# Optimization experiments

Hardware: AMD Instinct MI355X
Metric: run time of the kernel (lower is better)

## Reference

```python
import jax, jax.numpy as jnp
import numpy as np


def setup_inputs() -> dict:
    key = jax.random.key(0)
    kq, kk, kv = jax.random.split(key, 3)
    B, S, D = 16, 2048, 128
    q = jax.random.normal(kq, (B, S, D), dtype=jnp.float32)
    k = jax.random.normal(kk, (B, S, D), dtype=jnp.float32)
    v = jax.random.normal(kv, (B, S, D), dtype=jnp.float32)
    return {"q": q, "k": k, "v": v}


def reference(q, k, v):
    # scores = q @ k^T * scale  (scale = 1/sqrt(head_dim), the standard value
    # passed to this module; dropout=0.0 and attn_mask=None per defaults)
    scale = q.shape[-1] ** -0.5
    scores = jnp.einsum('bqd,bkd->bqk', q, k) * scale  # [B, S, S]
    attention = jax.nn.softmax(scores, axis=-1)
    context = jnp.einsum('bqk,bkd->bqd', attention, v)  # [B, S, D]
    return (context, attention)
```

## Files before the change

### kernel.cpp

```cpp
#include <hip/hip_runtime.h>

#define SS 2048
#define DD 128
#define NB 16
#define TM 64
#define TN 64
#define NITER (SS / TN)

typedef short bf16x8 __attribute__((ext_vector_type(8)));
typedef float f32x4 __attribute__((ext_vector_type(4)));

#define PSTRIDE 72

#define SL2E (0.08838834764831845f * 1.4426950408889634f)

__device__ __forceinline__ unsigned short f2bf(float x) {
    unsigned u = __builtin_bit_cast(unsigned, x);
    u += 0x7fffu + ((u >> 16) & 1u);
    return (unsigned short)(u >> 16);
}

__device__ __forceinline__ float fexp2(float x) {
#if __has_builtin(__builtin_amdgcn_exp2f)
    return __builtin_amdgcn_exp2f(x);
#else
    return __expf(x * 0.6931471805599453f);
#endif
}

#define LGKM0() asm volatile("s_waitcnt lgkmcnt(0)" ::: "memory")
#define BAR()   __builtin_amdgcn_s_barrier()

__global__ void prep_kernel(const float* __restrict__ k, const float* __restrict__ v,
                            unsigned short* __restrict__ kb, unsigned short* __restrict__ vt) {
    __shared__ unsigned short t[64 * 72];
    const int x = blockIdx.x, b = blockIdx.z, sb = blockIdx.y * 64;
    const int tid = threadIdx.x;
    if (x < 2) {
        const int db = x * 64;
        const int r16 = tid >> 4, c4 = (tid & 15) * 4;
        for (int i = 0; i < 4; ++i) {
            int sl = i * 16 + r16;
            float4 xx = *(const float4*)(v + ((size_t)(b * SS + sb + sl) * DD + db + c4));
            ushort4 u; u.x = f2bf(xx.x); u.y = f2bf(xx.y); u.z = f2bf(xx.z); u.w = f2bf(xx.w);
            *(ushort4*)&t[sl * 72 + c4] = u;
        }
        __syncthreads();
        for (int i = 0; i < 4; ++i) {
            int dl = i * 16 + r16;
            ushort4 u;
            u.x = t[(c4 + 0) * 72 + dl];
            u.y = t[(c4 + 1) * 72 + dl];
            u.z = t[(c4 + 2) * 72 + dl];
            u.w = t[(c4 + 3) * 72 + dl];
            *(ushort4*)(vt + ((size_t)(b * DD + db + dl) * SS + sb + c4)) = u;
        }
    } else {
        const int c0 = (x - 2) * 64;
        for (int i = 0; i < 4; ++i) {
            int e = i * 1024 + tid * 4;
            int r = e >> 6, c = e & 63;
            size_t off = (size_t)(b * SS + sb + r) * DD + c0 + c;
            float4 xx = *(const float4*)(k + off);
            ushort4 u; u.x = f2bf(xx.x); u.y = f2bf(xx.y); u.z = f2bf(xx.z); u.w = f2bf(xx.w);
            *(ushort4*)(kb + off) = u;
        }
    }
}

__global__ __launch_bounds__(512, 4)
void attn_kernel(const float* __restrict__ q,
                 const unsigned short* __restrict__ kb,
                 const unsigned short* __restrict__ vt,
                 float* __restrict__ attn, float* __restrict__ ctx) {
    __shared__ unsigned short P_lds[2][TM * PSTRIDE];
    __shared__ float rs_lds[TM];
    __shared__ float inv_lds[TM];

    const int tid = threadIdx.x;
    const int lane = tid & 63, w = tid >> 6;
    const int wm = w >> 2, wn = w & 3;
    const int l15 = lane & 15, quad = lane >> 4;

    const int bid = blockIdx.x;
    const int bb = ((bid & 7) << 1) | ((bid >> 3) & 1);
    const int q0 = (bid >> 4) * TM;

    if (tid < TM) rs_lds[tid] = 0.0f;

    bf16x8 qf[2][4];
    {
        const float* qg = q + ((size_t)(bb * SS + q0 + wm * 32 + l15)) * DD + quad * 8;
        for (int mi = 0; mi < 2; ++mi)
            for (int kk = 0; kk < 4; ++kk) {
                float4 a = *(const float4*)(qg + mi * 16 * DD + kk * 32);
                float4 b = *(const float4*)(qg + mi * 16 * DD + kk * 32 + 4);
                bf16x8 f;
                f[0] = (short)f2bf(a.x); f[1] = (short)f2bf(a.y);
                f[2] = (short)f2bf(a.z); f[3] = (short)f2bf(a.w);
                f[4] = (short)f2bf(b.x); f[5] = (short)f2bf(b.y);
                f[6] = (short)f2bf(b.z); f[7] = (short)f2bf(b.w);
                qf[mi][kk] = f;
            }
    }

    const unsigned short* kgb = kb + (size_t)bb * SS * DD;
    const unsigned short* vgb = vt + (size_t)bb * DD * SS;

    float rs[8];
    for (int j = 0; j < 8; ++j) rs[j] = 0.0f;
    {
        const unsigned short* kp = kgb + (size_t)(wn * 16 + l15) * DD + quad * 8;
#pragma unroll 2
        for (int it = 0; it < NITER; ++it) {
            f32x4 a0 = (f32x4){0.f, 0.f, 0.f, 0.f};
            f32x4 a1 = (f32x4){0.f, 0.f, 0.f, 0.f};
#pragma unroll
            for (int kk = 0; kk < 4; ++kk) {
                bf16x8 kf = *(const bf16x8*)(kp + kk * 32);
                a0 = __builtin_amdgcn_mfma_f32_16x16x32_bf16(qf[0][kk], kf, a0, 0, 0, 0);
                a1 = __builtin_amdgcn_mfma_f32_16x16x32_bf16(qf[1][kk], kf, a1, 0, 0, 0);
            }
#pragma unroll
            for (int r = 0; r < 4; ++r) {
                rs[r]     += fexp2(a0[r] * SL2E);
                rs[4 + r] += fexp2(a1[r] * SL2E);
            }
            kp += TN * DD;
        }
    }

#pragma unroll
    for (int j = 0; j < 8; ++j) {
        float s = rs[j];
        s += __shfl_xor(s, 1, 64);
        s += __shfl_xor(s, 2, 64);
        s += __shfl_xor(s, 4, 64);
        s += __shfl_xor(s, 8, 64);
        rs[j] = s;
    }
    __syncthreads();
    if (l15 == 0)
        for (int mi = 0; mi < 2; ++mi)
            for (int r = 0; r < 4; ++r)
                atomicAdd(&rs_lds[wm * 32 + mi * 16 + quad * 4 + r], rs[mi * 4 + r]);
    __syncthreads();
    if (tid < TM) inv_lds[tid] = 1.0f / rs_lds[tid];
    __syncthreads();
    float inv[2][4];
    for (int mi = 0; mi < 2; ++mi)
        for (int r = 0; r < 4; ++r)
            inv[mi][r] = inv_lds[wm * 32 + mi * 16 + quad * 4 + r];

    f32x4 cacc[2][2];
    for (int mi = 0; mi < 2; ++mi)
        for (int ni = 0; ni < 2; ++ni) cacc[mi][ni] = (f32x4){0.f, 0.f, 0.f, 0.f};

    float* ab = attn + (size_t)bb * SS * SS
              + (size_t)(q0 + wm * 32) * SS + (wn * 16 + l15);
    const unsigned short* kp0 = kgb + (size_t)(wn * 16 + l15) * DD + quad * 8;
    const unsigned short* vfp = vgb + (size_t)(wn * 32 + l15) * SS + quad * 8;

    bf16x8 kf[4];
#pragma unroll
    for (int kk = 0; kk < 4; ++kk) kf[kk] = *(const bf16x8*)(kp0 + kk * 32);
    const unsigned short* kpn = kp0 + (size_t)TN * DD;

    for (int it = 0; it < NITER; ++it) {
        const int k0 = it * TN;

        f32x4 acc[2];
        acc[0] = (f32x4){0.f, 0.f, 0.f, 0.f};
        acc[1] = (f32x4){0.f, 0.f, 0.f, 0.f};
        __builtin_amdgcn_s_setprio(1);
#pragma unroll
        for (int kk = 0; kk < 4; ++kk) {
            acc[0] = __builtin_amdgcn_mfma_f32_16x16x32_bf16(qf[0][kk], kf[kk], acc[0], 0, 0, 0);
            acc[1] = __builtin_amdgcn_mfma_f32_16x16x32_bf16(qf[1][kk], kf[kk], acc[1], 0, 0, 0);
        }
        __builtin_amdgcn_s_setprio(0);

        if (it < NITER - 1) {
#pragma unroll
            for (int kk = 0; kk < 4; ++kk) kf[kk] = *(const bf16x8*)(kpn + kk * 32);
            kpn += (size_t)TN * DD;
        }

        bf16x8 bv[2][2];
#pragma unroll
        for (int kk = 0; kk < 2; ++kk)
#pragma unroll
            for (int ni = 0; ni < 2; ++ni)
                bv[kk][ni] = *(const bf16x8*)(vfp + (size_t)(ni * 16) * SS + k0 + kk * 32);

        unsigned short* pw = &P_lds[it & 1][0];
#pragma unroll
        for (int mi = 0; mi < 2; ++mi)
#pragma unroll
            for (int r = 0; r < 4; ++r) {
                float p = fexp2(acc[mi][r] * SL2E) * inv[mi][r];
                __builtin_nontemporal_store(p, ab + (size_t)((mi * 16 + quad * 4 + r) * SS) + k0);
                pw[(wm * 32 + mi * 16 + quad * 4 + r) * PSTRIDE + wn * 16 + l15] = f2bf(p);
            }

        LGKM0();
        BAR();

        __builtin_amdgcn_s_setprio(1);
#pragma unroll
        for (int kk = 0; kk < 2; ++kk) {
            bf16x8 af0 = *(const bf16x8*)&pw[(wm * 32 +  0 + l15) * PSTRIDE + kk * 32 + quad * 8];
            bf16x8 af1 = *(const bf16x8*)&pw[(wm * 32 + 16 + l15) * PSTRIDE + kk * 32 + quad * 8];
            cacc[0][0] = __builtin_amdgcn_mfma_f32_16x16x32_bf16(af0, bv[kk][0], cacc[0][0], 0, 0, 0);
            cacc[1][0] = __builtin_amdgcn_mfma_f32_16x16x32_bf16(af1, bv[kk][0], cacc[1][0], 0, 0, 0);
            cacc[0][1] = __builtin_amdgcn_mfma_f32_16x16x32_bf16(af0, bv[kk][1], cacc[0][1], 0, 0, 0);
            cacc[1][1] = __builtin_amdgcn_mfma_f32_16x16x32_bf16(af1, bv[kk][1], cacc[1][1], 0, 0, 0);
        }
        __builtin_amdgcn_s_setprio(0);
    }

    float* cg = ctx + ((size_t)(bb * SS) + q0) * DD;
#pragma unroll
    for (int mi = 0; mi < 2; ++mi)
#pragma unroll
        for (int ni = 0; ni < 2; ++ni)
#pragma unroll
            for (int r = 0; r < 4; ++r) {
                int row = wm * 32 + mi * 16 + quad * 4 + r;
                int col = wn * 32 + ni * 16 + l15;
                __builtin_nontemporal_store(cacc[mi][ni][r], cg + (size_t)row * DD + col);
            }
}

extern "C" void kernel_launch(void* const* d_in, const int* in_sizes, int n_in,
                              void* d_out, int out_size, void* d_ws, size_t ws_size,
                              hipStream_t stream) {
    const float* q = (const float*)d_in[0];
    const float* k = (const float*)d_in[1];
    const float* v = (const float*)d_in[2];
    float* ctx = (float*)d_out;
    float* attn = ctx + (size_t)NB * SS * DD;

    unsigned short* kb = (unsigned short*)d_ws;
    unsigned short* vt = kb + (size_t)NB * SS * DD;

    prep_kernel<<<dim3(4, SS / 64, NB), 256, 0, stream>>>(k, v, kb, vt);
    attn_kernel<<<dim3((SS / TM) * NB), 512, 0, stream>>>(q, kb, vt, attn, ctx);
}
```

Baseline: 455.2 us.

## Stage K and V tiles into swizzled LDS via async global-to-LDS loads

K tiles, and V tiles in the second pass, are now cooperatively prefetched into XOR-swizzled shared memory buffers with global_load_lds. This replaces per-wave direct global loads, which duplicated K reads across the two wm wave rows. It adds a multi-buffered ring with vmcnt waits and an extra barrier per iteration. LDS use rises to about 64KB of K/V buffers, which may cut occupancy below the launch bound of 4 blocks. The P buffer also drops from double to single buffering.

```diff
diff --git a/kernel.cpp b/kernel.cpp
--- a/kernel.cpp
+++ b/kernel.cpp
@@ -28,8 +28,36 @@
 #endif
 }
 
-#define LGKM0() asm volatile("s_waitcnt lgkmcnt(0)" ::: "memory")
-#define BAR()   __builtin_amdgcn_s_barrier()
+#define LGKM0()    asm volatile("s_waitcnt lgkmcnt(0)" ::: "memory")
+#define VMCNT(n)   asm volatile("s_waitcnt vmcnt(" #n ")" ::: "memory")
+#define BAR()      __builtin_amdgcn_s_barrier()
+#define MEMFENCE() asm volatile("" ::: "memory")
+
+__device__ __forceinline__ void gld16(unsigned short* lds, const unsigned short* g) {
+    __builtin_amdgcn_global_load_lds(
+        (const __attribute__((address_space(1))) void*)g,
+        (__attribute__((address_space(3))) void*)lds, 16, 0, 0);
+}
+
+__device__ __forceinline__ void stage_k(unsigned short* buf, const unsigned short* kg, int tid) {
+#pragma unroll
+    for (int c = 0; c < 2; ++c) {
+        int e = c * 512 + tid;
+        int r = e >> 4;
+        int co = (e & 15) ^ (r & 7);
+        gld16(buf + e * 8, kg + (size_t)r * DD + co * 8);
+    }
+}
+
+__device__ __forceinline__ void stage_v(unsigned short* buf, const unsigned short* vg, int tid) {
+#pragma unroll
+    for (int c = 0; c < 2; ++c) {
+        int e = c * 512 + tid;
+        int r = e >> 3;
+        int co = (e & 7) ^ (r & 7);
+        gld16(buf + e * 8, vg + (size_t)r * SS + co * 8);
+    }
+}
 
 __global__ void prep_kernel(const float* __restrict__ k, const float* __restrict__ v,
                             unsigned short* __restrict__ kb, unsigned short* __restrict__ vt) {
@@ -73,7 +101,8 @@
                  const unsigned short* __restrict__ kb,
                  const unsigned short* __restrict__ vt,
                  float* __restrict__ attn, float* __restrict__ ctx) {
-    __shared__ unsigned short P_lds[2][TM * PSTRIDE];
+    __shared__ unsigned short KV[4][64 * 128];
+    __shared__ unsigned short P_lds[TM * PSTRIDE];
     __shared__ float rs_lds[TM];
     __shared__ float inv_lds[TM];
 
@@ -81,6 +110,7 @@
     const int lane = tid & 63, w = tid >> 6;
     const int wm = w >> 2, wn = w & 3;
     const int l15 = lane & 15, quad = lane >> 4;
+    const int sx = (l15 & 7) << 4;
 
     const int bid = blockIdx.x;
     const int bb = ((bid & 7) << 1) | ((bid >> 3) & 1);
@@ -106,28 +136,35 @@
 
     const unsigned short* kgb = kb + (size_t)bb * SS * DD;
     const unsigned short* vgb = vt + (size_t)bb * DD * SS;
+    const int rK = wn * 16 + l15;
 
     float rs[8];
     for (int j = 0; j < 8; ++j) rs[j] = 0.0f;
-    {
-        const unsigned short* kp = kgb + (size_t)(wn * 16 + l15) * DD + quad * 8;
-#pragma unroll 2
-        for (int it = 0; it < NITER; ++it) {
-            f32x4 a0 = (f32x4){0.f, 0.f, 0.f, 0.f};
-            f32x4 a1 = (f32x4){0.f, 0.f, 0.f, 0.f};
-#pragma unroll
-            for (int kk = 0; kk < 4; ++kk) {
-                bf16x8 kf = *(const bf16x8*)(kp + kk * 32);
-                a0 = __builtin_amdgcn_mfma_f32_16x16x32_bf16(qf[0][kk], kf, a0, 0, 0, 0);
-                a1 = __builtin_amdgcn_mfma_f32_16x16x32_bf16(qf[1][kk], kf, a1, 0, 0, 0);
-            }
-#pragma unroll
-            for (int r = 0; r < 4; ++r) {
-                rs[r]     += fexp2(a0[r] * SL2E);
-                rs[4 + r] += fexp2(a1[r] * SL2E);
-            }
-            kp += TN * DD;
-        }
+
+    stage_k(&KV[0][0], kgb, tid);
+    stage_k(&KV[1][0], kgb + (size_t)TN * DD, tid);
+    VMCNT(2);
+    BAR();
+
+    for (int it = 0; it < NITER; ++it) {
+        if (it + 2 < NITER)
+            stage_k(&KV[(it + 2) & 3][0], kgb + (size_t)(it + 2) * TN * DD, tid);
+        const char* kbuf = (const char*)&KV[it & 3][0];
+        f32x4 a0 = (f32x4){0.f, 0.f, 0.f, 0.f};
+        f32x4 a1 = (f32x4){0.f, 0.f, 0.f, 0.f};
+#pragma unroll
+        for (int kk = 0; kk < 4; ++kk) {
+            bf16x8 kf = *(const bf16x8*)(kbuf + rK * 256 + ((kk * 64 + quad * 16) ^ sx));
+            a0 = __builtin_amdgcn_mfma_f32_16x16x32_bf16(qf[0][kk], kf, a0, 0, 0, 0);
+            a1 = __builtin_amdgcn_mfma_f32_16x16x32_bf16(qf[1][kk], kf, a1, 0, 0, 0);
+        }
+#pragma unroll
+        for (int r = 0; r < 4; ++r) {
+            rs[r]     += fexp2(a0[r] * SL2E);
+            rs[4 + r] += fexp2(a1[r] * SL2E);
+        }
+        VMCNT(2);
+        BAR();
     }
 
 #pragma unroll
@@ -158,16 +195,22 @@
 
     float* ab = attn + (size_t)bb * SS * SS
               + (size_t)(q0 + wm * 32) * SS + (wn * 16 + l15);
-    const unsigned short* kp0 = kgb + (size_t)(wn * 16 + l15) * DD + quad * 8;
-    const unsigned short* vfp = vgb + (size_t)(wn * 32 + l15) * SS + quad * 8;
-
-    bf16x8 kf[4];
-#pragma unroll
-    for (int kk = 0; kk < 4; ++kk) kf[kk] = *(const bf16x8*)(kp0 + kk * 32);
-    const unsigned short* kpn = kp0 + (size_t)TN * DD;
+
+    stage_k(&KV[0][0], kgb, tid);
+    stage_v(&KV[2][0], vgb, tid);
+    VMCNT(0);
+    BAR();
 
     for (int it = 0; it < NITER; ++it) {
         const int k0 = it * TN;
+        if (it + 1 < NITER) {
+            stage_k(&KV[(it + 1) & 1][0], kgb + (size_t)(k0 + TN) * DD, tid);
+            stage_v(&KV[2 + ((it + 1) & 1)][0], vgb + (k0 + TN), tid);
+        }
+        MEMFENCE();
+
+        const char* kbuf = (const char*)&KV[it & 1][0];
+        const char* vbuf = (const char*)&KV[2 + (it & 1)][0];
 
         f32x4 acc[2];
         acc[0] = (f32x4){0.f, 0.f, 0.f, 0.f};
@@ -175,32 +218,19 @@
         __builtin_amdgcn_s_setprio(1);
 #pragma unroll
         for (int kk = 0; kk < 4; ++kk) {
-            acc[0] = __builtin_amdgcn_mfma_f32_16x16x32_bf16(qf[0][kk], kf[kk], acc[0], 0, 0, 0);
-            acc[1] = __builtin_amdgcn_mfma_f32_16x16x32_bf16(qf[1][kk], kf[kk], acc[1], 0, 0, 0);
+            bf16x8 kf = *(const bf16x8*)(kbuf + rK * 256 + ((kk * 64 + quad * 16) ^ sx));
+            acc[0] = __builtin_amdgcn_mfma_f32_16x16x32_bf16(qf[0][kk], kf, acc[0], 0, 0, 0);
+            acc[1] = __builtin_amdgcn_mfma_f32_16x16x32_bf16(qf[1][kk], kf, acc[1], 0, 0, 0);
         }
         __builtin_amdgcn_s_setprio(0);
 
-        if (it < NITER - 1) {
-#pragma unroll
-            for (int kk = 0; kk < 4; ++kk) kf[kk] = *(const bf16x8*)(kpn + kk * 32);
-            kpn += (size_t)TN * DD;
-        }
-
-        bf16x8 bv[2][2];
-#pragma unroll
-        for (int kk = 0; kk < 2; ++kk)
-#pragma unroll
-            for (int ni = 0; ni < 2; ++ni)
-                bv[kk][ni] = *(const bf16x8*)(vfp + (size_t)(ni * 16) * SS + k0 + kk * 32);
-
-        unsigned short* pw = &P_lds[it & 1][0];
 #pragma unroll
         for (int mi = 0; mi < 2; ++mi)
 #pragma unroll
             for (int r = 0; r < 4; ++r) {
                 float p = fexp2(acc[mi][r] * SL2E) * inv[mi][r];
                 __builtin_nontemporal_store(p, ab + (size_t)((mi * 16 + quad * 4 + r) * SS) + k0);
-                pw[(wm * 32 + mi * 16 + quad * 4 + r) * PSTRIDE + wn * 16 + l15] = f2bf(p);
+                P_lds[(wm * 32 + mi * 16 + quad * 4 + r) * PSTRIDE + wn * 16 + l15] = f2bf(p);
             }
 
         LGKM0();
@@ -209,14 +239,20 @@
         __builtin_amdgcn_s_setprio(1);
 #pragma unroll
         for (int kk = 0; kk < 2; ++kk) {
-            bf16x8 af0 = *(const bf16x8*)&pw[(wm * 32 +  0 + l15) * PSTRIDE + kk * 32 + quad * 8];
-            bf16x8 af1 = *(const bf16x8*)&pw[(wm * 32 + 16 + l15) * PSTRIDE + kk * 32 + quad * 8];
-            cacc[0][0] = __builtin_amdgcn_mfma_f32_16x16x32_bf16(af0, bv[kk][0], cacc[0][0], 0, 0, 0);
-            cacc[1][0] = __builtin_amdgcn_mfma_f32_16x16x32_bf16(af1, bv[kk][0], cacc[1][0], 0, 0, 0);
-            cacc[0][1] = __builtin_amdgcn_mfma_f32_16x16x32_bf16(af0, bv[kk][1], cacc[0][1], 0, 0, 0);
-            cacc[1][1] = __builtin_amdgcn_mfma_f32_16x16x32_bf16(af1, bv[kk][1], cacc[1][1], 0, 0, 0);
+            bf16x8 af0 = *(const bf16x8*)&P_lds[(wm * 32 +  0 + l15) * PSTRIDE + kk * 32 + quad * 8];
+            bf16x8 af1 = *(const bf16x8*)&P_lds[(wm * 32 + 16 + l15) * PSTRIDE + kk * 32 + quad * 8];
+            const int vc = kk * 64 + quad * 16;
+            bf16x8 bv0 = *(const bf16x8*)(vbuf + (wn * 32 +  0 + l15) * 128 + (vc ^ sx));
+            bf16x8 bv1 = *(const bf16x8*)(vbuf + (wn * 32 + 16 + l15) * 128 + (vc ^ sx));
+            cacc[0][0] = __builtin_amdgcn_mfma_f32_16x16x32_bf16(af0, bv0, cacc[0][0], 0, 0, 0);
+            cacc[1][0] = __builtin_amdgcn_mfma_f32_16x16x32_bf16(af1, bv0, cacc[1][0], 0, 0, 0);
+            cacc[0][1] = __builtin_amdgcn_mfma_f32_16x16x32_bf16(af0, bv1, cacc[0][1], 0, 0, 0);
+            cacc[1][1] = __builtin_amdgcn_mfma_f32_16x16x32_bf16(af1, bv1, cacc[1][1], 0, 0, 0);
         }
         __builtin_amdgcn_s_setprio(0);
+
+        VMCNT(8);
+        BAR();
     }
 
     float* cg = ctx + ((size_t)(bb * SS) + q0) * DD;
```

Result: faster. 375.5 us (-17.5%).
